# Kernel optimization log

Hardware: AMD Instinct MI355X
Metric: run time of the kernel (lower is better)

## Reference

```python
import jax, jax.numpy as jnp
import numpy as np

H = 64
NA, NB, NM, NC = 65536, 131072, 16384, 2048
EDGES = {  # name: (E, n_src, n_dst)
    'aa': (786432, NA, NA), 'ab': (262144, NA, NB), 'am': (262144, NA, NM),
    'bb': (786432, NB, NB), 'bm': (524288, NB, NM), 'mm': (131072, NM, NM),
    'ac': (65536,  NA, NC), 'bc': (131072, NB, NC), 'mc': (16384,  NM, NC),
}
REL_ORDER = ['aa', 'ab', 'am', 'bb', 'bm', 'mm', 'ac', 'bc', 'mc']
SRC = {'aa': 'atom', 'ab': 'atom', 'am': 'atom', 'bb': 'bond', 'bm': 'bond',
       'mm': 'motif', 'ac': 'atom', 'bc': 'bond', 'mc': 'motif'}
DST = {'aa': 'atom', 'ab': 'bond', 'am': 'motif', 'bb': 'bond', 'bm': 'motif',
       'mm': 'motif', 'ac': 'cell', 'bc': 'cell', 'mc': 'cell'}
SIZES = {'atom': NA, 'bond': NB, 'motif': NM, 'cell': NC}


def _edge(k, e, n_src, n_dst):
    k1, k2 = jax.random.split(k)
    return jnp.stack([jax.random.randint(k1, (e,), 0, n_src, dtype=jnp.int32),
                      jax.random.randint(k2, (e,), 0, n_dst, dtype=jnp.int32)])


def setup_inputs() -> dict:
    key = jax.random.key(0)
    ks = iter(jax.random.split(key, 32))
    s = 0.05
    inp = {
        'x_atom': jax.random.normal(next(ks), (NA, 92), jnp.float32),
        'x_bond': jax.random.normal(next(ks), (NB, 7), jnp.float32),
        'x_motif': jax.random.normal(next(ks), (NM, 35), jnp.float32),
        'x_cell': jax.random.normal(next(ks), (NC, H), jnp.float32),
        # input projections
        'Wa': jax.random.normal(next(ks), (92, H), jnp.float32) * s,
        'ba': jnp.zeros((H,), jnp.float32),
        'Wb': jax.random.normal(next(ks), (7, H), jnp.float32) * s,
        'bb_': jnp.zeros((H,), jnp.float32),
        'Wm': jax.random.normal(next(ks), (35, H), jnp.float32) * s,
        'bm_': jnp.zeros((H,), jnp.float32),
        # 9 CGConv relations, each lin_f/lin_s: [2H -> H]
        'Wf': jax.random.normal(next(ks), (9, 2 * H, H), jnp.float32) * s,
        'bf': jnp.zeros((9, H), jnp.float32),
        'Ws': jax.random.normal(next(ks), (9, 2 * H, H), jnp.float32) * s,
        'bs': jnp.zeros((9, H), jnp.float32),
        # head
        'Wp': jax.random.normal(next(ks), (H, H), jnp.float32) * s,
        'bp': jnp.zeros((H,), jnp.float32),
        'Wo': jax.random.normal(next(ks), (H, 1), jnp.float32) * s,
        'bo': jnp.zeros((1,), jnp.float32),
    }
    for name in REL_ORDER:
        e, ns, nd = EDGES[name]
        inp['e_' + name] = _edge(next(ks), e, ns, nd)
    return inp


def reference(x_atom, x_bond, x_motif, x_cell,
              Wa, ba, Wb, bb_, Wm, bm_, Wf, bf, Ws, bs, Wp, bp, Wo, bo,
              e_aa, e_ab, e_am, e_bb, e_bm, e_mm, e_ac, e_bc, e_mc):
    edges = {'aa': e_aa, 'ab': e_ab, 'am': e_am, 'bb': e_bb, 'bm': e_bm,
             'mm': e_mm, 'ac': e_ac, 'bc': e_bc, 'mc': e_mc}
    x = {'atom': x_atom @ Wa + ba,
         'bond': x_bond @ Wb + bb_,
         'motif': x_motif @ Wm + bm_,
         'cell': x_cell}
    # one HeteroConv layer (n_layers=1), aggr='sum' across relations per dst type
    new = {k: jnp.zeros_like(v) for k, v in x.items()}
    for r, name in enumerate(REL_ORDER):
        e = edges[name]
        src, dst = SRC[name], DST[name]
        xi = x[dst][e[1]]              # [E, H] target features (x_i)
        xj = x[src][e[0]]              # [E, H] source features (x_j)
        z = jnp.concatenate([xi, xj], axis=-1)  # [E, 2H]
        msg = jax.nn.sigmoid(z @ Wf[r] + bf[r]) * jax.nn.softplus(z @ Ws[r] + bs[r])
        agg = jax.ops.segment_sum(msg, e[1], num_segments=SIZES[dst])
        new[dst] = new[dst] + agg + x[dst]  # CGConv residual, summed over relations
    x = {k: jax.nn.relu(v) for k, v in new.items()}
    h = jax.nn.softplus(x['cell'] @ Wp + bp)
    return h @ Wo + bo  # [NC, 1]
```

## Files before the change

### kernel.cpp

```cpp
#include <hip/hip_runtime.h>
#include <hip/hip_fp16.h>

#define H 64
#define NA 65536
#define NB 131072
#define NM 16384
#define NC 2048
#define E_AC 65536
#define E_BC 131072
#define E_MC 16384
#define NE_TOT (E_AC + E_BC + E_MC)

#define CAPA 160
#define CAPB 224
#define CAPM 96
#define SLOTB (NC * CAPA)
#define SLOTM (SLOTB + NC * CAPB)
#define SLOT_TOT (SLOTM + NC * CAPM)

typedef __attribute__((ext_vector_type(8))) short bf16x8;
typedef __attribute__((ext_vector_type(4))) float f32x4;

__device__ __forceinline__ float sigmoidf_(float x) { return 1.0f / (1.0f + __expf(-x)); }
__device__ __forceinline__ float softplusf_(float x) {
    return fmaxf(x, 0.0f) + __logf(1.0f + __expf(-fabsf(x)));
}
__device__ __forceinline__ short bf16_of(float f) {
    union { float f; unsigned u; } v; v.f = f;
    unsigned r = (v.u + 0x7fff + ((v.u >> 16) & 1)) >> 16;
    return (short)r;
}

__global__ __launch_bounds__(256) void prep0_kernel(
    const float* __restrict__ Wa, const float* __restrict__ ba,
    const float* __restrict__ Wb, const float* __restrict__ bb_,
    const float* __restrict__ Wm, const float* __restrict__ bm,
    const float* __restrict__ Wf, const float* __restrict__ bf,
    const float* __restrict__ Ws, const float* __restrict__ bs,
    short* __restrict__ wpA, short* __restrict__ wpM, short* __restrict__ wpC,
    float* __restrict__ biasA, float* __restrict__ biasM, float* __restrict__ biasC,
    __half2* __restrict__ WcB, int* __restrict__ cnt)
{
    int b = blockIdx.x, tid = threadIdx.x;
    for (int i = b * 256 + tid; i < 3 * NC; i += gridDim.x * 256) cnt[i] = 0;

    if (b < 48) {
        int idx = b * 256 + tid;
        int k = idx >> 7, col = idx & 127, c = col & 63;
        const float* WB = ((col < 64) ? Wf : Ws) + (size_t)6 * 2 * H * H + (size_t)H * H;
        float v = 0.0f;
        if (k < 92) {
            const float* a = Wa + (size_t)k * H;
            for (int j = 0; j < H; ++j) v = fmaf(a[j], WB[j * H + c], v);
        }
        int t = col >> 4, lo = col & 15, sm = k >> 5, q = (k >> 3) & 3, e = k & 7;
        wpA[(size_t)(((t * 3 + sm) * 64) + q * 16 + lo) * 8 + e] = bf16_of(v);
    } else if (b < 80) {
        int idx = (b - 48) * 256 + tid;
        int k = idx >> 7, col = idx & 127, c = col & 63;
        const float* WB = ((col < 64) ? Wf : Ws) + (size_t)8 * 2 * H * H + (size_t)H * H;
        float v = 0.0f;
        if (k < 35) {
            const float* a = Wm + (size_t)k * H;
            for (int j = 0; j < H; ++j) v = fmaf(a[j], WB[j * H + c], v);
        }
        int t = col >> 4, lo = col & 15, sm = k >> 5, q = (k >> 3) & 3, e = k & 7;
        wpM[(size_t)(((t * 2 + sm) * 64) + q * 16 + lo) * 8 + e] = bf16_of(v);
    } else if (b < 176) {
        int cu = b - 80;
        int rel = cu >> 5;
        int idx = (cu & 31) * 256 + tid;
        int k = idx >> 7, col = idx & 127, c = col & 63;
        float v = ((col < 64) ? Wf : Ws)[(size_t)(6 + rel) * 2 * H * H + (size_t)k * H + c];
        int t = col >> 4, lo = col & 15, sm = k >> 5, q = (k >> 3) & 3, e = k & 7;
        wpC[(size_t)rel * 8192 + (size_t)(((t * 2 + sm) * 64) + q * 16 + lo) * 8 + e] = bf16_of(v);
    } else if (b == 176) {
        if (tid < 128) {
            int col = tid, c = col & 63;
            const float* WB = ((col < 64) ? Wf : Ws) + (size_t)6 * 2 * H * H + (size_t)H * H;
            float v = 0.0f;
            for (int j = 0; j < H; ++j) v = fmaf(ba[j], WB[j * H + c], v);
            biasA[col] = v;
        }
    } else if (b == 177) {
        if (tid < 128) {
            int col = tid, c = col & 63;
            const float* WB = ((col < 64) ? Wf : Ws) + (size_t)8 * 2 * H * H + (size_t)H * H;
            float v = 0.0f;
            for (int j = 0; j < H; ++j) v = fmaf(bm[j], WB[j * H + c], v);
            biasM[col] = v;
        }
    } else if (b == 178) {
        for (int i = tid; i < 384; i += 256) {
            int rel = i >> 7, col = i & 127, c = col & 63;
            biasC[rel * 128 + col] = ((col < 64) ? bf : bs)[(6 + rel) * H + c];
        }
    } else if (b < 181) {
        int idx = (b - 179) * 256 + tid;
        if (idx < 8 * 64) {
            int k = idx >> 6, col = idx & 63;
            const float* WfB = Wf + (size_t)7 * 2 * H * H + (size_t)H * H;
            const float* WsB = Ws + (size_t)7 * 2 * H * H + (size_t)H * H;
            const float* row = (k < 7) ? (Wb + (size_t)k * H) : bb_;
            float f = 0.0f, s = 0.0f;
            for (int j = 0; j < H; ++j) {
                float rv = row[j];
                f = fmaf(rv, WfB[j * H + col], f);
                s = fmaf(rv, WsB[j * H + col], s);
            }
            WcB[k * 64 + col] = __floats2half2_rn(f, s);
        }
    }
}

template<int K, int S, bool VEC>
__device__ __forceinline__ void gmfma_body(
    int blk, const float* __restrict__ x, const short* __restrict__ wp,
    const float* __restrict__ bias, __half2* __restrict__ g)
{
    int l = threadIdx.x & 63;
    int wv = threadIdx.x >> 6;
    int r0 = (blk * 4 + wv) * 16;
    int lrow = l & 15, q = l >> 4;

    float bF[4], bS[4];
    #pragma unroll
    for (int t = 0; t < 4; ++t) {
        bF[t] = bias[t * 16 + lrow];
        bS[t] = bias[64 + t * 16 + lrow];
    }

    f32x4 acc[8];
    #pragma unroll
    for (int t = 0; t < 8; ++t) acc[t] = (f32x4){0.f, 0.f, 0.f, 0.f};

    const float* xr = x + (size_t)(r0 + lrow) * K;
    #pragma unroll
    for (int s = 0; s < S; ++s) {
        int kb = s * 32 + q * 8;
        bf16x8 afrag;
        if (VEC && kb + 8 <= K) {
            float4 v0 = *(const float4*)(xr + kb);
            float4 v1 = *(const float4*)(xr + kb + 4);
            afrag[0] = bf16_of(v0.x); afrag[1] = bf16_of(v0.y);
            afrag[2] = bf16_of(v0.z); afrag[3] = bf16_of(v0.w);
            afrag[4] = bf16_of(v1.x); afrag[5] = bf16_of(v1.y);
            afrag[6] = bf16_of(v1.z); afrag[7] = bf16_of(v1.w);
        } else {
            #pragma unroll
            for (int e = 0; e < 8; ++e) {
                float xv = 0.0f;
                if (kb + e < K) xv = xr[kb + e];
                afrag[e] = bf16_of(xv);
            }
        }
        #pragma unroll
        for (int t = 0; t < 8; ++t) {
            bf16x8 bt = *(const bf16x8*)(wp + (size_t)((t * S + s) * 64 + l) * 8);
            acc[t] = __builtin_amdgcn_mfma_f32_16x16x32_bf16(afrag, bt, acc[t], 0, 0, 0);
        }
    }

    #pragma unroll
    for (int t = 0; t < 4; ++t)
        #pragma unroll
        for (int r = 0; r < 4; ++r) {
            float fv = acc[t][r] + bF[t];
            float sv = acc[t + 4][r] + bS[t];
            g[(size_t)(r0 + q * 4 + r) * H + t * 16 + lrow] = __floats2half2_rn(fv, sv);
        }
}

__global__ __launch_bounds__(256) void work_kernel(
    const float* __restrict__ xa, const float* __restrict__ xm, const float* __restrict__ xc,
    const short* __restrict__ wpA, const float* __restrict__ biasA,
    const short* __restrict__ wpM, const float* __restrict__ biasM,
    const short* __restrict__ wpC, const float* __restrict__ biasC,
    const int* __restrict__ ea, const int* __restrict__ eb, const int* __restrict__ em,
    int* __restrict__ cnt, int* __restrict__ slots,
    __half2* __restrict__ gA, __half2* __restrict__ gM, __half2* __restrict__ Ccomb)
{
    int b = blockIdx.x, tid = threadIdx.x;
    if (b < 104) {
        int t0 = b * 256 + tid;
        #pragma unroll
        for (int u2 = 0; u2 < 8; ++u2) {
            int i = t0 + u2 * 26624;
            int r, d, s;
            if (i < E_AC)             { r = 0; s = ea[i];                 d = ea[E_AC + i]; }
            else if (i < E_AC + E_BC) { int k = i - E_AC; r = 1; s = eb[k]; d = eb[E_BC + k]; }
            else                      { int k = i - E_AC - E_BC; r = 2; s = em[k]; d = em[E_MC + k]; }
            int pos = atomicAdd(&cnt[r * NC + d], 1);
            int base, cap;
            if (r == 0)      { base = d * CAPA;         cap = CAPA; }
            else if (r == 1) { base = SLOTB + d * CAPB; cap = CAPB; }
            else             { base = SLOTM + d * CAPM; cap = CAPM; }
            if (pos < cap) slots[base + pos] = s;
        }
    } else if (b < 200) {
        int cu = b - 104;
        int rel = cu >> 5, blk = cu & 31;
        gmfma_body<64, 2, true>(blk, xc, wpC + (size_t)rel * 8192, biasC + rel * 128,
                                Ccomb + (size_t)rel * NC * H);
    } else if (b < 456) {
        gmfma_body<35, 2, false>(b - 200, xm, wpM, biasM, gM);
    } else {
        gmfma_body<92, 3, true>(b - 456, xa, wpA, biasA, gA);
    }
}

__global__ __launch_bounds__(512) void cellacc_kernel(
    const __half2* __restrict__ gA, const __half2* __restrict__ gM,
    const float* __restrict__ xb, const __half2* __restrict__ WcB,
    const int* __restrict__ slots, const int* __restrict__ cnt,
    const __half2* __restrict__ Ccomb, const float* __restrict__ xc,
    const float* __restrict__ Wp, const float* __restrict__ bp,
    const float* __restrict__ Wo, const float* __restrict__ bo,
    float* __restrict__ out)
{
    __shared__ float red[8][H];
    __shared__ float vL[H];
    int d = blockIdx.x;
    int lane = threadIdx.x & 63, wv = threadIdx.x >> 6;
    float acc = 0.0f;

    {
        int n = min(cnt[d], CAPA);
        float2 cc = __half22float2(Ccomb[(size_t)d * H + lane]);
        const int* sl = slots + d * CAPA;
        for (int j = wv; j < n; j += 32) {
            float msk[4]; float2 av[4];
            #pragma unroll
            for (int v = 0; v < 4; ++v) {
                int jc = j + 8 * v;
                int jcs = __builtin_amdgcn_readfirstlane((jc < n) ? jc : (n - 1));
                int sidx = sl[jcs];
                msk[v] = (jc < n) ? 1.0f : 0.0f;
                av[v] = __half22float2(*(gA + (size_t)sidx * H + lane));
            }
            #pragma unroll
            for (int v = 0; v < 4; ++v)
                acc += msk[v] * (sigmoidf_(cc.x + av[v].x) * softplusf_(cc.y + av[v].y));
        }
    }
    {
        int n = min(cnt[NC + d], CAPB);
        float2 cc = __half22float2(Ccomb[(size_t)(NC + d) * H + lane]);
        float wcf[8], wcs[8];
        #pragma unroll
        for (int k = 0; k < 8; ++k) {
            float2 w = __half22float2(WcB[k * 64 + lane]);
            wcf[k] = w.x; wcs[k] = w.y;
        }
        const int* sl = slots + SLOTB + d * CAPB;
        for (int j = wv; j < n; j += 32) {
            float msk[4];
            float xr[4][7];
            #pragma unroll
            for (int v = 0; v < 4; ++v) {
                int jc = j + 8 * v;
                int jcs = __builtin_amdgcn_readfirstlane((jc < n) ? jc : (n - 1));
                int sidx = sl[jcs];
                msk[v] = (jc < n) ? 1.0f : 0.0f;
                const float* p = xb + (size_t)sidx * 7;
                #pragma unroll
                for (int k = 0; k < 7; ++k) xr[v][k] = p[k];
            }
            #pragma unroll
            for (int v = 0; v < 4; ++v) {
                float gf = wcf[7], gs = wcs[7];
                #pragma unroll
                for (int k = 0; k < 7; ++k) {
                    gf = fmaf(xr[v][k], wcf[k], gf);
                    gs = fmaf(xr[v][k], wcs[k], gs);
                }
                acc += msk[v] * (sigmoidf_(cc.x + gf) * softplusf_(cc.y + gs));
            }
        }
    }
    {
        int n = min(cnt[2 * NC + d], CAPM);
        float2 cc = __half22float2(Ccomb[(size_t)(2 * NC + d) * H + lane]);
        const int* sl = slots + SLOTM + d * CAPM;
        for (int j = wv; j < n; j += 32) {
            float msk[4]; float2 av[4];
            #pragma unroll
            for (int v = 0; v < 4; ++v) {
                int jc = j + 8 * v;
                int jcs = __builtin_amdgcn_readfirstlane((jc < n) ? jc : (n - 1));
                int sidx = sl[jcs];
                msk[v] = (jc < n) ? 1.0f : 0.0f;
                av[v] = __half22float2(*(gM + (size_t)sidx * H + lane));
            }
            #pragma unroll
            for (int v = 0; v < 4; ++v)
                acc += msk[v] * (sigmoidf_(cc.x + av[v].x) * softplusf_(cc.y + av[v].y));
        }
    }

    red[wv][lane] = acc;
    __syncthreads();
    if (wv == 0) {
        float a = 3.0f * xc[(size_t)d * H + lane];
        #pragma unroll
        for (int w = 0; w < 8; ++w) a += red[w][lane];
        vL[lane] = fmaxf(a, 0.0f);
        __builtin_amdgcn_s_waitcnt(0);
        float aj = bp[lane];
        #pragma unroll
        for (int k = 0; k < H; ++k) aj = fmaf(vL[k], Wp[k * H + lane], aj);
        float contrib = softplusf_(aj) * Wo[lane];
        #pragma unroll
        for (int o = 32; o > 0; o >>= 1) contrib += __shfl_down(contrib, o, 64);
        if (lane == 0) out[d] = contrib + bo[0];
    }
}

extern "C" void kernel_launch(void* const* d_in, const int* in_sizes, int n_in,
                              void* d_out, int out_size, void* d_ws, size_t ws_size,
                              hipStream_t stream)
{
    const float* xa = (const float*)d_in[0];
    const float* xb = (const float*)d_in[1];
    const float* xm = (const float*)d_in[2];
    const float* xc = (const float*)d_in[3];
    const float* Wa = (const float*)d_in[4];
    const float* ba = (const float*)d_in[5];
    const float* Wb = (const float*)d_in[6];
    const float* bb_ = (const float*)d_in[7];
    const float* Wm = (const float*)d_in[8];
    const float* bm = (const float*)d_in[9];
    const float* Wf = (const float*)d_in[10];
    const float* bf = (const float*)d_in[11];
    const float* Ws = (const float*)d_in[12];
    const float* bs = (const float*)d_in[13];
    const float* Wp = (const float*)d_in[14];
    const float* bp = (const float*)d_in[15];
    const float* Wo = (const float*)d_in[16];
    const float* bo = (const float*)d_in[17];
    const int* ea = (const int*)d_in[24];
    const int* eb = (const int*)d_in[25];
    const int* em = (const int*)d_in[26];

    char* base = (char*)d_ws;
    size_t o = 0;
    auto alloc = [&](size_t bytes) { char* r = base + o; o = (o + bytes + 255) & ~(size_t)255; return r; };
    int*     cnt   = (int*)    alloc(3 * NC * sizeof(int));
    int*     slots = (int*)    alloc(SLOT_TOT * sizeof(int));
    short*   wpA   = (short*)  alloc(8 * 3 * 64 * 8 * sizeof(short));
    short*   wpM   = (short*)  alloc(8 * 2 * 64 * 8 * sizeof(short));
    short*   wpC   = (short*)  alloc(3 * 8192 * sizeof(short));
    float*   biasA = (float*)  alloc(128 * sizeof(float));
    float*   biasM = (float*)  alloc(128 * sizeof(float));
    float*   biasC = (float*)  alloc(384 * sizeof(float));
    __half2* WcB   = (__half2*)alloc(8 * 64 * sizeof(__half2));
    __half2* Ccomb = (__half2*)alloc((size_t)3 * NC * H * sizeof(__half2));
    __half2* gA    = (__half2*)alloc((size_t)NA * H * sizeof(__half2));
    __half2* gM    = (__half2*)alloc((size_t)NM * H * sizeof(__half2));
    float*   out   = (float*)d_out;

    prep0_kernel<<<181, 256, 0, stream>>>(Wa, ba, Wb, bb_, Wm, bm, Wf, bf, Ws, bs,
                                          wpA, wpM, wpC, biasA, biasM, biasC, WcB, cnt);
    work_kernel<<<1480, 256, 0, stream>>>(xa, xm, xc, wpA, biasA, wpM, biasM, wpC, biasC,
                                          ea, eb, em, cnt, slots, gA, gM, Ccomb);
    cellacc_kernel<<<NC, 512, 0, stream>>>(gA, gM, xb, WcB, slots, cnt, Ccomb,
                                           xc, Wp, bp, Wo, bo, out);
}
```

Measured before the change: 78.51 us.

## Precompute bond gate projections densely and unify cell accumulation over one slot list

New measurement: 70.95 us. 9.6% less time.

```diff
diff --git a/kernel.cpp b/kernel.cpp
--- a/kernel.cpp
+++ b/kernel.cpp
@@ -37,9 +37,10 @@
     const float* __restrict__ Wm, const float* __restrict__ bm,
     const float* __restrict__ Wf, const float* __restrict__ bf,
     const float* __restrict__ Ws, const float* __restrict__ bs,
-    short* __restrict__ wpA, short* __restrict__ wpM, short* __restrict__ wpC,
-    float* __restrict__ biasA, float* __restrict__ biasM, float* __restrict__ biasC,
-    __half2* __restrict__ WcB, int* __restrict__ cnt)
+    short* __restrict__ wpA, short* __restrict__ wpM, short* __restrict__ wpB,
+    short* __restrict__ wpC,
+    float* __restrict__ biasA, float* __restrict__ biasM, float* __restrict__ biasB,
+    float* __restrict__ biasC, int* __restrict__ cnt)
 {
     int b = blockIdx.x, tid = threadIdx.x;
     for (int i = b * 256 + tid; i < 3 * NC; i += gridDim.x * 256) cnt[i] = 0;
@@ -74,7 +75,18 @@
         float v = ((col < 64) ? Wf : Ws)[(size_t)(6 + rel) * 2 * H * H + (size_t)k * H + c];
         int t = col >> 4, lo = col & 15, sm = k >> 5, q = (k >> 3) & 3, e = k & 7;
         wpC[(size_t)rel * 8192 + (size_t)(((t * 2 + sm) * 64) + q * 16 + lo) * 8 + e] = bf16_of(v);
-    } else if (b == 176) {
+    } else if (b < 192) {
+        int idx = (b - 176) * 256 + tid;
+        int k = idx >> 7, col = idx & 127, c = col & 63;
+        const float* WB = ((col < 64) ? Wf : Ws) + (size_t)7 * 2 * H * H + (size_t)H * H;
+        float v = 0.0f;
+        if (k < 7) {
+            const float* a = Wb + (size_t)k * H;
+            for (int j = 0; j < H; ++j) v = fmaf(a[j], WB[j * H + c], v);
+        }
+        int t = col >> 4, lo = col & 15, q = (k >> 3) & 3, e = k & 7;
+        wpB[(size_t)((t * 64) + q * 16 + lo) * 8 + e] = bf16_of(v);
+    } else if (b == 192) {
         if (tid < 128) {
             int col = tid, c = col & 63;
             const float* WB = ((col < 64) ? Wf : Ws) + (size_t)6 * 2 * H * H + (size_t)H * H;
@@ -82,7 +94,7 @@
             for (int j = 0; j < H; ++j) v = fmaf(ba[j], WB[j * H + c], v);
             biasA[col] = v;
         }
-    } else if (b == 177) {
+    } else if (b == 193) {
         if (tid < 128) {
             int col = tid, c = col & 63;
             const float* WB = ((col < 64) ? Wf : Ws) + (size_t)8 * 2 * H * H + (size_t)H * H;
@@ -90,25 +102,18 @@
             for (int j = 0; j < H; ++j) v = fmaf(bm[j], WB[j * H + c], v);
             biasM[col] = v;
         }
-    } else if (b == 178) {
+    } else if (b == 194) {
+        if (tid < 128) {
+            int col = tid, c = col & 63;
+            const float* WB = ((col < 64) ? Wf : Ws) + (size_t)7 * 2 * H * H + (size_t)H * H;
+            float v = 0.0f;
+            for (int j = 0; j < H; ++j) v = fmaf(bb_[j], WB[j * H + c], v);
+            biasB[col] = v;
+        }
+    } else {
         for (int i = tid; i < 384; i += 256) {
             int rel = i >> 7, col = i & 127, c = col & 63;
             biasC[rel * 128 + col] = ((col < 64) ? bf : bs)[(6 + rel) * H + c];
-        }
-    } else if (b < 181) {
-        int idx = (b - 179) * 256 + tid;
-        if (idx < 8 * 64) {
-            int k = idx >> 6, col = idx & 63;
-            const float* WfB = Wf + (size_t)7 * 2 * H * H + (size_t)H * H;
-            const float* WsB = Ws + (size_t)7 * 2 * H * H + (size_t)H * H;
-            const float* row = (k < 7) ? (Wb + (size_t)k * H) : bb_;
-            float f = 0.0f, s = 0.0f;
-            for (int j = 0; j < H; ++j) {
-                float rv = row[j];
-                f = fmaf(rv, WfB[j * H + col], f);
-                s = fmaf(rv, WsB[j * H + col], s);
-            }
-            WcB[k * 64 + col] = __floats2half2_rn(f, s);
         }
     }
 }
@@ -172,13 +177,15 @@
 }
 
 __global__ __launch_bounds__(256) void work_kernel(
-    const float* __restrict__ xa, const float* __restrict__ xm, const float* __restrict__ xc,
+    const float* __restrict__ xa, const float* __restrict__ xb, const float* __restrict__ xm,
+    const float* __restrict__ xc,
     const short* __restrict__ wpA, const float* __restrict__ biasA,
     const short* __restrict__ wpM, const float* __restrict__ biasM,
+    const short* __restrict__ wpB, const float* __restrict__ biasB,
     const short* __restrict__ wpC, const float* __restrict__ biasC,
     const int* __restrict__ ea, const int* __restrict__ eb, const int* __restrict__ em,
     int* __restrict__ cnt, int* __restrict__ slots,
-    __half2* __restrict__ gA, __half2* __restrict__ gM, __half2* __restrict__ Ccomb)
+    __half2* __restrict__ gAll, __half2* __restrict__ Ccomb)
 {
     int b = blockIdx.x, tid = threadIdx.x;
     if (b < 104) {
@@ -187,9 +194,9 @@
         for (int u2 = 0; u2 < 8; ++u2) {
             int i = t0 + u2 * 26624;
             int r, d, s;
-            if (i < E_AC)             { r = 0; s = ea[i];                 d = ea[E_AC + i]; }
-            else if (i < E_AC + E_BC) { int k = i - E_AC; r = 1; s = eb[k]; d = eb[E_BC + k]; }
-            else                      { int k = i - E_AC - E_BC; r = 2; s = em[k]; d = em[E_MC + k]; }
+            if (i < E_AC)             { r = 0; s = ea[i];                      d = ea[E_AC + i]; }
+            else if (i < E_AC + E_BC) { int k = i - E_AC; r = 1; s = NA + eb[k]; d = eb[E_BC + k]; }
+            else                      { int k = i - E_AC - E_BC; r = 2; s = NA + NB + em[k]; d = em[E_MC + k]; }
             int pos = atomicAdd(&cnt[r * NC + d], 1);
             int base, cap;
             if (r == 0)      { base = d * CAPA;         cap = CAPA; }
@@ -202,100 +209,59 @@
         int rel = cu >> 5, blk = cu & 31;
         gmfma_body<64, 2, true>(blk, xc, wpC + (size_t)rel * 8192, biasC + rel * 128,
                                 Ccomb + (size_t)rel * NC * H);
-    } else if (b < 456) {
-        gmfma_body<35, 2, false>(b - 200, xm, wpM, biasM, gM);
+    } else if (b < 1224) {
+        gmfma_body<92, 3, true>(b - 200, xa, wpA, biasA, gAll);
+    } else if (b < 3272) {
+        gmfma_body<7, 1, false>(b - 1224, xb, wpB, biasB, gAll + (size_t)NA * H);
     } else {
-        gmfma_body<92, 3, true>(b - 456, xa, wpA, biasA, gA);
+        gmfma_body<35, 2, false>(b - 3272, xm, wpM, biasM, gAll + (size_t)(NA + NB) * H);
     }
 }
 
 __global__ __launch_bounds__(512) void cellacc_kernel(
-    const __half2* __restrict__ gA, const __half2* __restrict__ gM,
-    const float* __restrict__ xb, const __half2* __restrict__ WcB,
+    const __half2* __restrict__ gAll,
     const int* __restrict__ slots, const int* __restrict__ cnt,
     const __half2* __restrict__ Ccomb, const float* __restrict__ xc,
     const float* __restrict__ Wp, const float* __restrict__ bp,
     const float* __restrict__ Wo, const float* __restrict__ bo,
     float* __restrict__ out)
 {
+    __shared__ int   sL[CAPA + CAPB + CAPM];
     __shared__ float red[8][H];
     __shared__ float vL[H];
     int d = blockIdx.x;
-    int lane = threadIdx.x & 63, wv = threadIdx.x >> 6;
+    int tid = threadIdx.x, lane = tid & 63, wv = tid >> 6;
+
+    int nA = min(cnt[d], CAPA);
+    int nB = min(cnt[NC + d], CAPB);
+    int nM = min(cnt[2 * NC + d], CAPM);
+    for (int i = tid; i < nA; i += 512) sL[i] = slots[d * CAPA + i];
+    for (int i = tid; i < nB; i += 512) sL[nA + i] = slots[SLOTB + d * CAPB + i];
+    for (int i = tid; i < nM; i += 512) sL[nA + nB + i] = slots[SLOTM + d * CAPM + i];
+    float2 ccA = __half22float2(Ccomb[(size_t)d * H + lane]);
+    float2 ccB = __half22float2(Ccomb[(size_t)(NC + d) * H + lane]);
+    float2 ccM = __half22float2(Ccomb[(size_t)(2 * NC + d) * H + lane]);
+    __syncthreads();
+
+    int ntot = nA + nB + nM, nAB = nA + nB;
     float acc = 0.0f;
-
-    {
-        int n = min(cnt[d], CAPA);
-        float2 cc = __half22float2(Ccomb[(size_t)d * H + lane]);
-        const int* sl = slots + d * CAPA;
-        for (int j = wv; j < n; j += 32) {
-            float msk[4]; float2 av[4];
-            #pragma unroll
-            for (int v = 0; v < 4; ++v) {
-                int jc = j + 8 * v;
-                int jcs = __builtin_amdgcn_readfirstlane((jc < n) ? jc : (n - 1));
-                int sidx = sl[jcs];
-                msk[v] = (jc < n) ? 1.0f : 0.0f;
-                av[v] = __half22float2(*(gA + (size_t)sidx * H + lane));
-            }
-            #pragma unroll
-            for (int v = 0; v < 4; ++v)
-                acc += msk[v] * (sigmoidf_(cc.x + av[v].x) * softplusf_(cc.y + av[v].y));
-        }
-    }
-    {
-        int n = min(cnt[NC + d], CAPB);
-        float2 cc = __half22float2(Ccomb[(size_t)(NC + d) * H + lane]);
-        float wcf[8], wcs[8];
-        #pragma unroll
-        for (int k = 0; k < 8; ++k) {
-            float2 w = __half22float2(WcB[k * 64 + lane]);
-            wcf[k] = w.x; wcs[k] = w.y;
-        }
-        const int* sl = slots + SLOTB + d * CAPB;
-        for (int j = wv; j < n; j += 32) {
-            float msk[4];
-            float xr[4][7];
-            #pragma unroll
-            for (int v = 0; v < 4; ++v) {
-                int jc = j + 8 * v;
-                int jcs = __builtin_amdgcn_readfirstlane((jc < n) ? jc : (n - 1));
-                int sidx = sl[jcs];
-                msk[v] = (jc < n) ? 1.0f : 0.0f;
-                const float* p = xb + (size_t)sidx * 7;
-                #pragma unroll
-                for (int k = 0; k < 7; ++k) xr[v][k] = p[k];
-            }
-            #pragma unroll
-            for (int v = 0; v < 4; ++v) {
-                float gf = wcf[7], gs = wcs[7];
-                #pragma unroll
-                for (int k = 0; k < 7; ++k) {
-                    gf = fmaf(xr[v][k], wcf[k], gf);
-                    gs = fmaf(xr[v][k], wcs[k], gs);
-                }
-                acc += msk[v] * (sigmoidf_(cc.x + gf) * softplusf_(cc.y + gs));
-            }
-        }
-    }
-    {
-        int n = min(cnt[2 * NC + d], CAPM);
-        float2 cc = __half22float2(Ccomb[(size_t)(2 * NC + d) * H + lane]);
-        const int* sl = slots + SLOTM + d * CAPM;
-        for (int j = wv; j < n; j += 32) {
-            float msk[4]; float2 av[4];
-            #pragma unroll
-            for (int v = 0; v < 4; ++v) {
-                int jc = j + 8 * v;
-                int jcs = __builtin_amdgcn_readfirstlane((jc < n) ? jc : (n - 1));
-                int sidx = sl[jcs];
-                msk[v] = (jc < n) ? 1.0f : 0.0f;
-                av[v] = __half22float2(*(gM + (size_t)sidx * H + lane));
-            }
-            #pragma unroll
-            for (int v = 0; v < 4; ++v)
-                acc += msk[v] * (sigmoidf_(cc.x + av[v].x) * softplusf_(cc.y + av[v].y));
-        }
+    int cs = (ntot + 7) >> 3;
+    int p0 = wv * cs, p1 = min(p0 + cs, ntot);
+    for (int p = p0; p < p1; p += 4) {
+        float ccx[4], ccy[4], msk[4]; float2 av[4];
+        #pragma unroll
+        for (int v = 0; v < 4; ++v) {
+            int pc = p + v;
+            msk[v] = (pc < p1) ? 1.0f : 0.0f;
+            pc = min(pc, ntot - 1);
+            int row = sL[pc];
+            ccx[v] = (pc < nA) ? ccA.x : (pc < nAB) ? ccB.x : ccM.x;
+            ccy[v] = (pc < nA) ? ccA.y : (pc < nAB) ? ccB.y : ccM.y;
+            av[v] = __half22float2(gAll[(size_t)row * H + lane]);
+        }
+        #pragma unroll
+        for (int v = 0; v < 4; ++v)
+            acc += msk[v] * (sigmoidf_(ccx[v] + av[v].x) * softplusf_(ccy[v] + av[v].y));
     }
 
     red[wv][lane] = acc;
@@ -349,20 +315,22 @@
     int*     slots = (int*)    alloc(SLOT_TOT * sizeof(int));
     short*   wpA   = (short*)  alloc(8 * 3 * 64 * 8 * sizeof(short));
     short*   wpM   = (short*)  alloc(8 * 2 * 64 * 8 * sizeof(short));
+    short*   wpB   = (short*)  alloc(8 * 1 * 64 * 8 * sizeof(short));
     short*   wpC   = (short*)  alloc(3 * 8192 * sizeof(short));
     float*   biasA = (float*)  alloc(128 * sizeof(float));
     float*   biasM = (float*)  alloc(128 * sizeof(float));
+    float*   biasB = (float*)  alloc(128 * sizeof(float));
     float*   biasC = (float*)  alloc(384 * sizeof(float));
-    __half2* WcB   = (__half2*)alloc(8 * 64 * sizeof(__half2));
     __half2* Ccomb = (__half2*)alloc((size_t)3 * NC * H * sizeof(__half2));
-    __half2* gA    = (__half2*)alloc((size_t)NA * H * sizeof(__half2));
-    __half2* gM    = (__half2*)alloc((size_t)NM * H * sizeof(__half2));
+    __half2* gAll  = (__half2*)alloc((size_t)(NA + NB + NM) * H * sizeof(__half2));
     float*   out   = (float*)d_out;
 
-    prep0_kernel<<<181, 256, 0, stream>>>(Wa, ba, Wb, bb_, Wm, bm, Wf, bf, Ws, bs,
-                                          wpA, wpM, wpC, biasA, biasM, biasC, WcB, cnt);
-    work_kernel<<<1480, 256, 0, stream>>>(xa, xm, xc, wpA, biasA, wpM, biasM, wpC, biasC,
-                                          ea, eb, em, cnt, slots, gA, gM, Ccomb);
-    cellacc_kernel<<<NC, 512, 0, stream>>>(gA, gM, xb, WcB, slots, cnt, Ccomb,
+    prep0_kernel<<<196, 256, 0, stream>>>(Wa, ba, Wb, bb_, Wm, bm, Wf, bf, Ws, bs,
+                                          wpA, wpM, wpB, wpC,
+                                          biasA, biasM, biasB, biasC, cnt);
+    work_kernel<<<3528, 256, 0, stream>>>(xa, xb, xm, xc,
+                                          wpA, biasA, wpM, biasM, wpB, biasB, wpC, biasC,
+                                          ea, eb, em, cnt, slots, gAll, Ccomb);
+    cellacc_kernel<<<NC, 512, 0, stream>>>(gAll, slots, cnt, Ccomb,
                                            xc, Wp, bp, Wo, bo, out);
 }
```
